# Performance work log

Measured on AMD Instinct MI355X. Metric: run time of the kernel, lower is better.

The kernel has to match this reference:

```python
import jax, jax.numpy as jnp
import numpy as np

HEADS = 8
HEAD_DIM = 64
DIM = HEADS * HEAD_DIM  # 512
K = 7  # kernel_size (square)


def setup_inputs() -> dict:
    key = jax.random.key(0)
    ks = jax.random.split(key, 5)
    B, H, W = 1, 80, 80
    x = jax.random.normal(ks[0], (B, H, W, DIM), jnp.float32)
    qkv_w = jax.random.normal(ks[1], (3 * DIM, DIM), jnp.float32) * 0.02
    qkv_b = jnp.zeros((3 * DIM,), jnp.float32)
    rpb = jax.random.normal(ks[2], (HEADS, 2 * K - 1, 2 * K - 1), jnp.float32) * 0.02
    proj_w = jax.random.normal(ks[3], (DIM, DIM), jnp.float32) * 0.02
    proj_b = jnp.zeros((DIM,), jnp.float32)
    return {"x": x, "qkv_w": qkv_w, "qkv_b": qkv_b, "rpb": rpb,
            "proj_w": proj_w, "proj_b": proj_b}


def _window_indices(L, k):
    # NATTEN-style clamped neighborhood: window of size k fully in-bounds,
    # centered at the query when possible.
    starts = jnp.clip(jnp.arange(L) - k // 2, 0, L - k)          # [L]
    idx = starts[:, None] + jnp.arange(k)[None, :]               # [L, k] neighbor coords
    off = idx - jnp.arange(L)[:, None] + (k - 1)                 # [L, k] rpb index in [0, 2k-2]
    return idx, off


def reference(x, qkv_w, qkv_b, rpb, proj_w, proj_b):
    B, H, W, C = x.shape
    n, hd, k = HEADS, HEAD_DIM, K

    qkv = (x @ qkv_w.T + qkv_b).reshape(B, H, W, 3, n, hd)
    qkv = qkv.transpose(3, 0, 4, 1, 2, 5)                        # [3,B,n,H,W,hd]
    q, kk, v = qkv[0], qkv[1], qkv[2]
    q = q * (hd ** -0.5)

    idx_h, off_h = _window_indices(H, k)                         # [H,k]
    idx_w, off_w = _window_indices(W, k)                         # [W,k]

    # Gather neighborhood windows: [B,n,H,k,W,k,hd]
    k_nb = kk[:, :, idx_h][:, :, :, :, idx_w]
    v_nb = v[:, :, idx_h][:, :, :, :, idx_w]

    # attn logits: q[b,n,i,j,d] . k_nb[b,n,i,a,j,c,d] -> [B,n,H,W,k,k]
    attn = jnp.einsum('bnijd,bniajcd->bnijac', q, k_nb)

    # relative position bias: rpb[h, off_h[i,a], off_w[j,c]] -> [n,H,k,W,k]
    bias = rpb[:, off_h[:, :, None, None], off_w[None, None, :, :]]
    attn = attn + bias.transpose(0, 1, 3, 2, 4)[None]            # -> [1,n,H,W,k,k]

    a = jax.nn.softmax(attn.reshape(B, n, H, W, k * k), axis=-1)
    a = a.reshape(B, n, H, W, k, k)

    out = jnp.einsum('bnijac,bniajcd->bnijd', a, v_nb)           # [B,n,H,W,hd]
    out = out.transpose(0, 2, 3, 1, 4).reshape(B, H, W, C)
    out = out @ proj_w.T + proj_b
    return out
```

## Files before the change

kernel.cpp:

```cpp
#include <hip/hip_runtime.h>
#include <hip/hip_bf16.h>


typedef __attribute__((ext_vector_type(4))) float f32x4;
typedef __attribute__((ext_vector_type(8))) short bf16x8;
typedef __attribute__((ext_vector_type(4))) short s16x4;

#define HEADS 8
#define HEAD_DIM 64
#define DIM 512
#define KW 7
#define HH 80
#define WW 80
#define NPIX (HH * WW)

__device__ inline unsigned short f2bf(float f) {
    union { __hip_bfloat16 b; unsigned short u; } cvt;
    cvt.b = __float2bfloat16(f);
    return cvt.u;
}
__device__ inline float bf2f(short s) {
    union { float f; unsigned u; } c;
    c.u = ((unsigned)(unsigned short)s) << 16;
    return c.f;
}

__device__ inline void storeC(float* p, float v) { *p = v; }
__device__ inline void storeC(__hip_bfloat16* p, float v) { *p = __float2bfloat16(v); }

__device__ inline void g2l16(const void* g, void* l) {
    __builtin_amdgcn_global_load_lds(
        (const __attribute__((address_space(1))) unsigned int*)g,
        (__attribute__((address_space(3))) unsigned int*)l,
        16, 0, 0);
}

__global__ __launch_bounds__(256) void cast3_f32_bf16(
    const float* __restrict__ a, short* __restrict__ oa, int na4,
    const float* __restrict__ b, short* __restrict__ ob, int nb4,
    const float* __restrict__ c, short* __restrict__ oc, int nc4)
{
    int i = blockIdx.x * 256 + threadIdx.x;
    const float* src; short* dst; int idx;
    if (i < na4) { src = a; dst = oa; idx = i; }
    else if (i < na4 + nb4) { src = b; dst = ob; idx = i - na4; }
    else if (i < na4 + nb4 + nc4) { src = c; dst = oc; idx = i - na4 - nb4; }
    else return;
    f32x4 v = reinterpret_cast<const f32x4*>(src)[idx];
    s16x4 r;
#pragma unroll
    for (int j = 0; j < 4; ++j) r[j] = (short)f2bf(v[j]);
    reinterpret_cast<s16x4*>(dst)[idx] = r;
}

template <int BM, int BN, typename CT>
__global__ __launch_bounds__(256) void gemm_sb(
    const __hip_bfloat16* __restrict__ A,
    const __hip_bfloat16* __restrict__ W,
    const float* __restrict__ bias,
    CT* __restrict__ C,
    int M, int N, int K)
{
    constexpr int WM = BM / 2, WN = BN / 2;
    constexpr int MI = WM / 16, NI = WN / 16;
    __shared__ __align__(16) short lds[(BM + BN) * 64];
    short* sA = lds;
    short* sB2 = lds + BM * 64;

    const int tid = threadIdx.x;
    const int lane = tid & 63;
    const int wv = tid >> 6;
    const int wr = wv >> 1;
    const int wc = wv & 1;
    const int r0 = blockIdx.y * BM;
    const int c0 = blockIdx.x * BN;
    const int rf = lane & 15;
    const int kg = lane >> 4;
    const int NT = K >> 6;

    auto stage = [&](const __hip_bfloat16* src, int rowbase, int kb,
                     short* dst, int ntasks) {
        for (int q = 0; q < ntasks / 256; ++q) {
            const int L = q * 256 + tid;
            const int r = L >> 3;
            const int cs = (L & 7) ^ (r & 7);
            g2l16(src + (size_t)(rowbase + r) * K + kb + cs * 8, dst + (size_t)L * 8);
        }
    };
    auto frag = [&](const short* base, int row, int ch) -> bf16x8 {
        return *reinterpret_cast<const bf16x8*>(base + row * 64 + ((ch ^ (row & 7)) << 3));
    };

    f32x4 acc[MI][NI] = {};

    for (int t = 0; t < NT; ++t) {
        stage(A, r0, t * 64, sA, BM * 8);
        stage(W, c0, t * 64, sB2, BN * 8);
        __syncthreads();
#pragma unroll
        for (int ks = 0; ks < 2; ++ks) {
            bf16x8 af[MI], bfr[NI];
#pragma unroll
            for (int i = 0; i < MI; ++i)
                af[i] = frag(sA, wr * WM + i * 16 + rf, ks * 4 + kg);
#pragma unroll
            for (int j = 0; j < NI; ++j)
                bfr[j] = frag(sB2, wc * WN + j * 16 + rf, ks * 4 + kg);
#pragma unroll
            for (int i = 0; i < MI; ++i)
#pragma unroll
                for (int j = 0; j < NI; ++j)
                    acc[i][j] = __builtin_amdgcn_mfma_f32_16x16x32_bf16(af[i], bfr[j], acc[i][j], 0, 0, 0);
        }
        __syncthreads();
    }

#pragma unroll
    for (int j = 0; j < NI; ++j) {
        const int col = c0 + wc * WN + j * 16 + rf;
        const float bcol = bias[col];
#pragma unroll
        for (int i = 0; i < MI; ++i) {
#pragma unroll
            for (int r = 0; r < 4; ++r) {
                const int row = r0 + wr * WM + i * 16 + kg * 4 + r;
                storeC(C + (size_t)row * N + col, acc[i][j][r] + bcol);
            }
        }
    }
}

__global__ __launch_bounds__(256, 3) void natten_mfma(
    const __hip_bfloat16* __restrict__ qkv,
    const float* __restrict__ rpb,
    __hip_bfloat16* __restrict__ aout)
{
    __shared__ __align__(16) short reg1[13312];
    __shared__ __align__(16) short reg2[13312];
    short* sK  = reg1;
    short* sP  = reg1;
    short* sQ  = reg2;
    float* sB  = (float*)(reg2 + 4096);
    short* sVT = reg2;

    const int tid = threadIdx.x;
    const int lane = tid & 63;
    const int wv = tid >> 6;
    const int l15 = lane & 15;
    const int kg = lane >> 4;
    const int h = blockIdx.y;
    const int ti = blockIdx.x / 10;
    const int tj = blockIdx.x - ti * 10;
    const int R0 = ti * 8 - 3;
    const int C0 = tj * 8 - 3;

    if (tid < 169) sB[tid] = rpb[h * 169 + tid];

#pragma unroll
    for (int i = 0; i < 2; ++i) {
        const int L = i * 256 + tid;
        const int row = L >> 3, ch = L & 7;
        const int pi = ti * 8 + (row >> 3), pjg = tj * 8 + (row & 7);
        const int cs = ch ^ (row & 7);
        g2l16(qkv + ((size_t)(pi * WW + pjg) * 1536 + h * 64 + cs * 8),
              sQ + (size_t)L * 8);
    }
#pragma unroll
    for (int i = 0; i < 7; ++i) {
        const int t = i * 256 + tid;
        if (t < 1568) {
            const int slot = t >> 3, ch = t & 7;
            const int r = slot / 14, c = slot - r * 14;
            int gi = R0 + r; gi = gi < 0 ? 0 : (gi > 79 ? 79 : gi);
            int gj = C0 + c; gj = gj < 0 ? 0 : (gj > 79 ? 79 : gj);
            const int cs = ch ^ (slot & 7);
            g2l16(qkv + ((size_t)(gi * WW + gj) * 1536 + 512 + h * 64 + cs * 8),
                  sK + (size_t)t * 8);
        }
    }
    __syncthreads();

    bf16x8 vbuf[7];
#pragma unroll
    for (int i = 0; i < 7; ++i) {
        const int t = i * 256 + tid;
        if (t < 1568) {
            const int slot = t % 196, ch = t / 196;
            const int r = slot / 14, c = slot - r * 14;
            int gi = R0 + r; gi = gi < 0 ? 0 : (gi > 79 ? 79 : gi);
            int gj = C0 + c; gj = gj < 0 ? 0 : (gj > 79 ? 79 : gj);
            vbuf[i] = *reinterpret_cast<const bf16x8*>(
                qkv + ((size_t)(gi * WW + gj) * 1536 + 1024 + h * 64 + ch * 8));
        }
    }

    auto fragswz = [&](const short* base, int row, int ch) -> bf16x8 {
        return *reinterpret_cast<const bf16x8*>(base + row * 64 + ((ch ^ (row & 7)) << 3));
    };

    f32x4 acc[13];
#pragma unroll
    for (int nt = 0; nt < 13; ++nt) acc[nt] = f32x4{0.f, 0.f, 0.f, 0.f};
    {
        bf16x8 aq0 = fragswz(sQ, wv * 16 + l15, kg);
        bf16x8 aq1 = fragswz(sQ, wv * 16 + l15, 4 + kg);
#pragma unroll
        for (int nt = 0; nt < 13; ++nt) {
            bf16x8 bk0 = fragswz(sK, nt * 16 + l15, kg);
            bf16x8 bk1 = fragswz(sK, nt * 16 + l15, 4 + kg);
            acc[nt] = __builtin_amdgcn_mfma_f32_16x16x32_bf16(aq0, bk0, acc[nt], 0, 0, 0);
            acc[nt] = __builtin_amdgcn_mfma_f32_16x16x32_bf16(aq1, bk1, acc[nt], 0, 0, 0);
        }
    }

    int pil[4], pjl[4], sil[4], sjl[4];
#pragma unroll
    for (int rg = 0; rg < 4; ++rg) {
        const int px = wv * 16 + kg * 4 + rg;
        const int pl = px >> 3, pw = px & 7;
        const int pi = ti * 8 + pl, pjg = tj * 8 + pw;
        int si = pi - 3; si = si < 0 ? 0 : (si > 73 ? 73 : si);
        int sj = pjg - 3; sj = sj < 0 ? 0 : (sj > 73 ? 73 : sj);
        pil[rg] = pl; pjl[rg] = pw;
        sil[rg] = si - R0; sjl[rg] = sj - C0;
    }
    float m4[4] = {-1e30f, -1e30f, -1e30f, -1e30f};
#pragma unroll
    for (int nt = 0; nt < 13; ++nt) {
        const int slot = nt * 16 + l15;
        const int r = slot / 14, c = slot - (slot / 14) * 14;
        const bool sv = slot < 196;
#pragma unroll
        for (int rg = 0; rg < 4; ++rg) {
            const unsigned a = (unsigned)(r - sil[rg]);
            const unsigned b = (unsigned)(c - sjl[rg]);
            float lv = -1e30f;
            if (sv && a < 7u && b < 7u)
                lv = 0.125f * acc[nt][rg] +
                     sB[(r - pil[rg] + 3) * 13 + (c - pjl[rg] + 3)];
            acc[nt][rg] = lv;
            m4[rg] = fmaxf(m4[rg], lv);
        }
    }
#pragma unroll
    for (int rg = 0; rg < 4; ++rg) {
        m4[rg] = fmaxf(m4[rg], __shfl_xor(m4[rg], 1, 64));
        m4[rg] = fmaxf(m4[rg], __shfl_xor(m4[rg], 2, 64));
        m4[rg] = fmaxf(m4[rg], __shfl_xor(m4[rg], 4, 64));
        m4[rg] = fmaxf(m4[rg], __shfl_xor(m4[rg], 8, 64));
    }
    float s4[4] = {0.f, 0.f, 0.f, 0.f};
#pragma unroll
    for (int nt = 0; nt < 13; ++nt)
#pragma unroll
        for (int rg = 0; rg < 4; ++rg) {
            const float e = __expf(acc[nt][rg] - m4[rg]);
            acc[nt][rg] = e;
            s4[rg] += e;
        }
#pragma unroll
    for (int rg = 0; rg < 4; ++rg) {
        s4[rg] += __shfl_xor(s4[rg], 1, 64);
        s4[rg] += __shfl_xor(s4[rg], 2, 64);
        s4[rg] += __shfl_xor(s4[rg], 4, 64);
        s4[rg] += __shfl_xor(s4[rg], 8, 64);
    }
    float rs[4];
#pragma unroll
    for (int rg = 0; rg < 4; ++rg) rs[rg] = 1.0f / s4[rg];

    __syncthreads();

#pragma unroll
    for (int nt = 0; nt < 13; ++nt) {
        const int slot = nt * 16 + l15;
#pragma unroll
        for (int rg = 0; rg < 4; ++rg) {
            const int px = wv * 16 + kg * 4 + rg;
            sP[px * 208 + slot] = (short)f2bf(acc[nt][rg]);
        }
    }
#pragma unroll
    for (int i = 0; i < 7; ++i) {
        const int t = i * 256 + tid;
        if (t < 1568) {
            const int slot = t % 196, ch = t / 196;
#pragma unroll
            for (int j = 0; j < 8; ++j)
                sVT[(ch * 8 + j) * 208 + slot] = vbuf[i][j];
        }
    }
#pragma unroll
    for (int i = 0; i < 3; ++i) {
        const int idx = i * 256 + tid;
        if (idx < 768) sVT[(idx / 12) * 208 + 196 + (idx - (idx / 12) * 12)] = 0;
    }
    __syncthreads();

    f32x4 oacc[4];
#pragma unroll
    for (int nt = 0; nt < 4; ++nt) oacc[nt] = f32x4{0.f, 0.f, 0.f, 0.f};
#pragma unroll
    for (int ks = 0; ks < 6; ++ks) {
        bf16x8 ap = *reinterpret_cast<const bf16x8*>(
            sP + (wv * 16 + l15) * 208 + (ks * 4 + kg) * 8);
#pragma unroll
        for (int nt = 0; nt < 4; ++nt) {
            bf16x8 bv = *reinterpret_cast<const bf16x8*>(
                sVT + (nt * 16 + l15) * 208 + (ks * 4 + kg) * 8);
            oacc[nt] = __builtin_amdgcn_mfma_f32_16x16x32_bf16(ap, bv, oacc[nt], 0, 0, 0);
        }
    }
#pragma unroll
    for (int s = 192; s < 196; ++s) {
        float pw[4];
#pragma unroll
        for (int rg = 0; rg < 4; ++rg)
            pw[rg] = bf2f(sP[(wv * 16 + kg * 4 + rg) * 208 + s]);
#pragma unroll
        for (int nt = 0; nt < 4; ++nt) {
            const float vv = bf2f(sVT[(nt * 16 + l15) * 208 + s]);
#pragma unroll
            for (int rg = 0; rg < 4; ++rg)
                oacc[nt][rg] += pw[rg] * vv;
        }
    }

#pragma unroll
    for (int rg = 0; rg < 4; ++rg) {
        const int px = wv * 16 + kg * 4 + rg;
        const int pi = ti * 8 + (px >> 3), pjg = tj * 8 + (px & 7);
        __hip_bfloat16* dst = aout + (size_t)(pi * WW + pjg) * 512 + h * 64;
        const float rsv = rs[rg];
#pragma unroll
        for (int nt = 0; nt < 4; ++nt)
            dst[nt * 16 + l15] = __float2bfloat16(oacc[nt][rg] * rsv);
    }
}

extern "C" void kernel_launch(void* const* d_in, const int* in_sizes, int n_in,
                              void* d_out, int out_size, void* d_ws, size_t ws_size,
                              hipStream_t stream) {
    const float* x      = (const float*)d_in[0];
    const float* qkv_w  = (const float*)d_in[1];
    const float* qkv_b  = (const float*)d_in[2];
    const float* rpb    = (const float*)d_in[3];
    const float* proj_w = (const float*)d_in[4];
    const float* proj_b = (const float*)d_in[5];
    float* out = (float*)d_out;

    char* wsb = (char*)d_ws;
    __hip_bfloat16* xb    = (__hip_bfloat16*)wsb;
    __hip_bfloat16* wqkv  = (__hip_bfloat16*)(wsb + 6553600);
    __hip_bfloat16* wproj = (__hip_bfloat16*)(wsb + 8126464);
    __hip_bfloat16* qkv   = (__hip_bfloat16*)(wsb + 8650752);
    __hip_bfloat16* aout  = (__hip_bfloat16*)(wsb + 28311552);

    dim3 blk(256);
    cast3_f32_bf16<<<dim3((819200 + 196608 + 65536 + 255) / 256), blk, 0, stream>>>(
        x, (short*)xb, 819200, qkv_w, (short*)wqkv, 196608, proj_w, (short*)wproj, 65536);

    gemm_sb<64, 128, __hip_bfloat16><<<dim3((3 * DIM) / 128, NPIX / 64), blk, 0, stream>>>(
        xb, wqkv, qkv_b, qkv, NPIX, 3 * DIM, DIM);

    natten_mfma<<<dim3(100, 8), blk, 0, stream>>>(qkv, rpb, aout);

    gemm_sb<64, 64, float><<<dim3(DIM / 64, NPIX / 64), blk, 0, stream>>>(
        aout, wproj, proj_b, out, NPIX, DIM, DIM);
}
```

Before: 126.6 us.

## Double-buffer GEMM LDS tiles and remap blocks across XCDs

Both GEMMs now use two LDS buffers and prefetch the next K-tile with async global-to-LDS loads while the current tile is consumed by MFMA, using explicit vmcnt waits and raw barriers instead of __syncthreads. The 2D grid becomes a 1D grid whose block index is permuted so that consecutive tiles land on the same XCD, for better L2 locality. This doubles LDS use per block, which may reduce occupancy, and the hand-written waitcnt must match the number of issued loads.

```diff
diff --git a/kernel.cpp b/kernel.cpp
--- a/kernel.cpp
+++ b/kernel.cpp
@@ -54,65 +54,80 @@
 }
 
 template <int BM, int BN, typename CT>
-__global__ __launch_bounds__(256) void gemm_sb(
+__global__ __launch_bounds__(256) void gemm_db(
     const __hip_bfloat16* __restrict__ A,
     const __hip_bfloat16* __restrict__ W,
     const float* __restrict__ bias,
     CT* __restrict__ C,
-    int M, int N, int K)
+    int M, int N, int K, int gxn)
 {
     constexpr int WM = BM / 2, WN = BN / 2;
     constexpr int MI = WM / 16, NI = WN / 16;
-    __shared__ __align__(16) short lds[(BM + BN) * 64];
-    short* sA = lds;
-    short* sB2 = lds + BM * 64;
+    constexpr int TASKS = (BM + BN) / 32;
+    __shared__ __align__(16) short lds[2][(BM + BN) * 64];
+
+    const int cpx = gridDim.x >> 3;
+    const int w = (blockIdx.x & 7) * cpx + (blockIdx.x >> 3);
+    const int r0 = (w / gxn) * BM;
+    const int c0 = (w % gxn) * BN;
 
     const int tid = threadIdx.x;
     const int lane = tid & 63;
     const int wv = tid >> 6;
     const int wr = wv >> 1;
     const int wc = wv & 1;
-    const int r0 = blockIdx.y * BM;
-    const int c0 = blockIdx.x * BN;
     const int rf = lane & 15;
     const int kg = lane >> 4;
     const int NT = K >> 6;
 
-    auto stage = [&](const __hip_bfloat16* src, int rowbase, int kb,
-                     short* dst, int ntasks) {
-        for (int q = 0; q < ntasks / 256; ++q) {
+    auto stage = [&](int t, int buf) {
+#pragma unroll
+        for (int q = 0; q < TASKS; ++q) {
             const int L = q * 256 + tid;
             const int r = L >> 3;
             const int cs = (L & 7) ^ (r & 7);
-            g2l16(src + (size_t)(rowbase + r) * K + kb + cs * 8, dst + (size_t)L * 8);
+            const __hip_bfloat16* src =
+                (r < BM) ? A + (size_t)(r0 + r) * K + t * 64 + cs * 8
+                         : W + (size_t)(c0 + (r - BM)) * K + t * 64 + cs * 8;
+            g2l16(src, &lds[buf][(size_t)L * 8]);
         }
     };
-    auto frag = [&](const short* base, int row, int ch) -> bf16x8 {
-        return *reinterpret_cast<const bf16x8*>(base + row * 64 + ((ch ^ (row & 7)) << 3));
+    auto frag = [&](int buf, int row, int ch) -> bf16x8 {
+        return *reinterpret_cast<const bf16x8*>(
+            &lds[buf][row * 64 + ((ch ^ (row & 7)) << 3)]);
     };
 
     f32x4 acc[MI][NI] = {};
 
+    stage(0, 0);
     for (int t = 0; t < NT; ++t) {
-        stage(A, r0, t * 64, sA, BM * 8);
-        stage(W, c0, t * 64, sB2, BN * 8);
-        __syncthreads();
+        const int buf = t & 1;
+        if (t + 1 < NT) {
+            stage(t + 1, buf ^ 1);
+            asm volatile("s_waitcnt vmcnt(%0)" :: "n"(TASKS) : "memory");
+        } else {
+            asm volatile("s_waitcnt vmcnt(0)" ::: "memory");
+        }
+        __builtin_amdgcn_sched_barrier(0);
+        __builtin_amdgcn_s_barrier();
+        __builtin_amdgcn_sched_barrier(0);
 #pragma unroll
         for (int ks = 0; ks < 2; ++ks) {
             bf16x8 af[MI], bfr[NI];
 #pragma unroll
             for (int i = 0; i < MI; ++i)
-                af[i] = frag(sA, wr * WM + i * 16 + rf, ks * 4 + kg);
+                af[i] = frag(buf, wr * WM + i * 16 + rf, ks * 4 + kg);
 #pragma unroll
             for (int j = 0; j < NI; ++j)
-                bfr[j] = frag(sB2, wc * WN + j * 16 + rf, ks * 4 + kg);
+                bfr[j] = frag(buf, BM + wc * WN + j * 16 + rf, ks * 4 + kg);
 #pragma unroll
             for (int i = 0; i < MI; ++i)
 #pragma unroll
                 for (int j = 0; j < NI; ++j)
                     acc[i][j] = __builtin_amdgcn_mfma_f32_16x16x32_bf16(af[i], bfr[j], acc[i][j], 0, 0, 0);
         }
-        __syncthreads();
+        __builtin_amdgcn_sched_barrier(0);
+        __builtin_amdgcn_s_barrier();
     }
 
 #pragma unroll
@@ -360,11 +375,11 @@
     cast3_f32_bf16<<<dim3((819200 + 196608 + 65536 + 255) / 256), blk, 0, stream>>>(
         x, (short*)xb, 819200, qkv_w, (short*)wqkv, 196608, proj_w, (short*)wproj, 65536);
 
-    gemm_sb<64, 128, __hip_bfloat16><<<dim3((3 * DIM) / 128, NPIX / 64), blk, 0, stream>>>(
-        xb, wqkv, qkv_b, qkv, NPIX, 3 * DIM, DIM);
+    gemm_db<64, 128, __hip_bfloat16><<<dim3(1200), blk, 0, stream>>>(
+        xb, wqkv, qkv_b, qkv, NPIX, 3 * DIM, DIM, 12);
 
     natten_mfma<<<dim3(100, 8), blk, 0, stream>>>(qkv, rpb, aout);
 
-    gemm_sb<64, 64, float><<<dim3(DIM / 64, NPIX / 64), blk, 0, stream>>>(
-        aout, wproj, proj_b, out, NPIX, DIM, DIM);
-}
+    gemm_db<64, 64, float><<<dim3(800), blk, 0, stream>>>(
+        aout, wproj, proj_b, out, NPIX, DIM, DIM, 8);
+}
```

Measured after the change: 121.9 us. 1.04x faster.
